# Performance work log

Hardware: AMD Instinct MI355X
Metric: run time of the kernel (lower is better)

Reference implementation:

```python
import jax, jax.numpy as jnp
import numpy as np

NUM_HEADS = 16
HIDDEN = 1024
EPS = 1e-5


def _layer_norm(x, g, b):
    m = jnp.mean(x, axis=-1, keepdims=True)
    v = jnp.mean(jnp.square(x - m), axis=-1, keepdims=True)
    return (x - m) * jax.lax.rsqrt(v + EPS) * g + b


def setup_inputs() -> dict:
    key = jax.random.key(0)
    ks = jax.random.split(key, 6)
    B, S, H = 2, 2048, HIDDEN
    x = jax.random.normal(ks[0], (B, S, H), dtype=jnp.float32)
    # True = masked (original passes ~attn_mask to SDPA); causal mask
    causal = ~jnp.tril(jnp.ones((S, S), dtype=bool))
    attn_mask = causal[None, None, :, :]  # [1,1,S,S]
    sc = 1.0 / np.sqrt(H)
    qkv_w = jax.random.normal(ks[1], (H, 3 * H), dtype=jnp.float32) * sc
    qkv_b = jnp.zeros((3 * H,), dtype=jnp.float32)
    out_w = jax.random.normal(ks[2], (H, H), dtype=jnp.float32) * sc
    out_b = jnp.zeros((H,), dtype=jnp.float32)
    w1 = jax.random.normal(ks[3], (H, 4 * H), dtype=jnp.float32) * sc
    b1 = jnp.zeros((4 * H,), dtype=jnp.float32)
    w2 = jax.random.normal(ks[4], (4 * H, H), dtype=jnp.float32) * (1.0 / np.sqrt(4 * H))
    b2 = jnp.zeros((H,), dtype=jnp.float32)
    return {
        'x': x, 'attn_mask': attn_mask,
        'qkv_w': qkv_w, 'qkv_b': qkv_b, 'out_w': out_w, 'out_b': out_b,
        'w1': w1, 'b1': b1, 'w2': w2, 'b2': b2,
        'ln1_g': jnp.ones((H,), jnp.float32), 'ln1_b': jnp.zeros((H,), jnp.float32),
        'ln2_g': jnp.ones((H,), jnp.float32), 'ln2_b': jnp.zeros((H,), jnp.float32),
    }


def reference(x, attn_mask, qkv_w, qkv_b, out_w, out_b, w1, b1, w2, b2,
              ln1_g, ln1_b, ln2_g, ln2_b):
    B, S, H = x.shape
    nh = NUM_HEADS
    hd = H // nh
    qkv = x @ qkv_w + qkv_b                      # [B,S,3H]
    q, k, v = jnp.split(qkv, 3, axis=-1)
    q = q.reshape(B, S, nh, hd).transpose(0, 2, 1, 3)  # [B,nh,S,hd]
    k = k.reshape(B, S, nh, hd).transpose(0, 2, 1, 3)
    v = v.reshape(B, S, nh, hd).transpose(0, 2, 1, 3)
    scores = jnp.einsum('bhqd,bhkd->bhqk', q, k) / jnp.sqrt(jnp.asarray(hd, x.dtype))
    scores = jnp.where(attn_mask, jnp.finfo(scores.dtype).min, scores)
    p = jax.nn.softmax(scores, axis=-1)
    attn = jnp.einsum('bhqk,bhkd->bhqd', p, v)   # [B,nh,S,hd]
    attn = attn.transpose(0, 2, 1, 3).reshape(B, S, H)
    attn = attn @ out_w + out_b
    x = _layer_norm(x + attn, ln1_g, ln1_b)
    h = jax.nn.relu(x @ w1 + b1) @ w2 + b2
    x = _layer_norm(x + h, ln2_g, ln2_b)
    return x
```

## Files before the change

### kernel.cpp

```cpp
#include <hip/hip_runtime.h>
#include <hip/hip_bf16.h>

typedef __bf16 bf16x8 __attribute__((ext_vector_type(8)));
typedef __bf16 bf16x4 __attribute__((ext_vector_type(4)));
typedef float f32x4 __attribute__((ext_vector_type(4)));

__device__ __forceinline__ void gload16(void* lds, const void* g) {
  __builtin_amdgcn_global_load_lds((const __attribute__((address_space(1))) void*)g,
                                   (__attribute__((address_space(3))) void*)lds, 16, 0, 0);
}

__global__ __launch_bounds__(256)
void transpose_cast(const float* __restrict__ in, __bf16* __restrict__ out, int R, int C)
{
  __shared__ __bf16 tile[32][33];
  const int bc = blockIdx.x * 32, br = blockIdx.y * 32;
  const int lx = threadIdx.x & 31, ly = threadIdx.x >> 5;
#pragma unroll
  for (int p = 0; p < 4; ++p)
    tile[ly + p * 8][lx] = (__bf16)in[(size_t)(br + ly + p * 8) * C + bc + lx];
  __syncthreads();
#pragma unroll
  for (int p = 0; p < 4; ++p)
    out[(size_t)(bc + ly + p * 8) * R + br + lx] = tile[lx][ly + p * 8];
}

__global__ __launch_bounds__(256)
void vtrans(const __bf16* __restrict__ qkv, __bf16* __restrict__ vtg)
{
  __shared__ __bf16 tile[32][33];
  const int sx = blockIdx.x * 32;
  const int dy = blockIdx.y * 32;
  const int z = blockIdx.z;
  const int b = z >> 4, h = z & 15;
  const int lx = threadIdx.x & 31, ly = threadIdx.x >> 5;
  const __bf16* src = qkv + (size_t)b * 2048 * 3072 + 2048 + h * 64;
#pragma unroll
  for (int p = 0; p < 4; ++p)
    tile[ly + p * 8][lx] = src[(size_t)(sx + ly + p * 8) * 3072 + dy + lx];
  __syncthreads();
  __bf16* dst = vtg + (size_t)z * 64 * 2048;
#pragma unroll
  for (int p = 0; p < 4; ++p)
    dst[(size_t)(dy + ly + p * 8) * 2048 + sx + lx] = tile[lx][ly + p * 8];
}

__global__ __launch_bounds__(256)
void cast_bf16(const float* __restrict__ in, __bf16* __restrict__ out)
{
  const int i = (blockIdx.x * 256 + threadIdx.x) * 4;
  float4 v = *(const float4*)(in + i);
  out[i] = (__bf16)v.x; out[i + 1] = (__bf16)v.y;
  out[i + 2] = (__bf16)v.z; out[i + 3] = (__bf16)v.w;
}

template<int BN, bool OUT_BF16, bool RELU, bool RESID>
__global__ __launch_bounds__(256)
void gemm_bt(const __bf16* __restrict__ A, const __bf16* __restrict__ Bt,
             const float* __restrict__ bias, const float* __restrict__ resid,
             void* __restrict__ Cv, int M, int N, int K)
{
  constexpr int NW = BN / 32;
  __shared__ __bf16 As[2][128 * 64];
  __shared__ __bf16 Bs[2][BN * 64];
  const int tid = threadIdx.x;
  const int wave = tid >> 6, lane = tid & 63;
  const int g = lane >> 4, l16 = lane & 15;
  const int row0 = blockIdx.x * 128, col0 = blockIdx.y * BN;
  const int wr = wave >> 1, wc = wave & 1;
  f32x4 acc[4][NW] = {};
  const int nk = K >> 6;

  auto STAGE = [&](int buf, int k0) {
#pragma unroll
    for (int r = 0; r < 4; ++r) {
      const int seg = r * 256 + tid;
      const int arow = seg >> 3;
      const int ko = ((seg & 7) ^ (arow & 7)) * 8;
      gload16(&As[buf][(r * 256 + wave * 64) * 8], &A[(size_t)(row0 + arow) * K + k0 + ko]);
    }
#pragma unroll
    for (int r = 0; r < BN / 32; ++r) {
      const int seg = r * 256 + tid;
      const int brow = seg >> 3;
      const int ko = ((seg & 7) ^ (brow & 7)) * 8;
      gload16(&Bs[buf][(r * 256 + wave * 64) * 8], &Bt[(size_t)(col0 + brow) * K + k0 + ko]);
    }
  };

  STAGE(0, 0);
  __syncthreads();
  int cur = 0;
  for (int t = 0; t < nk; ++t) {
    if (t + 1 < nk) STAGE(cur ^ 1, (t + 1) << 6);
#pragma unroll
    for (int kk = 0; kk < 2; ++kk) {
      bf16x8 af[4], bfr[NW];
#pragma unroll
      for (int m = 0; m < 4; ++m) {
        const int row = wr * 64 + m * 16 + l16;
        af[m] = *(const bf16x8*)&As[cur][row * 64 + ((kk * 32 + g * 8) ^ ((row & 7) << 3))];
      }
#pragma unroll
      for (int n = 0; n < NW; ++n) {
        const int row = wc * (BN / 2) + n * 16 + l16;
        bfr[n] = *(const bf16x8*)&Bs[cur][row * 64 + ((kk * 32 + g * 8) ^ ((row & 7) << 3))];
      }
#pragma unroll
      for (int m = 0; m < 4; ++m)
#pragma unroll
        for (int n = 0; n < NW; ++n)
          acc[m][n] = __builtin_amdgcn_mfma_f32_16x16x32_bf16(af[m], bfr[n], acc[m][n], 0, 0, 0);
    }
    __syncthreads();
    cur ^= 1;
  }
#pragma unroll
  for (int n = 0; n < NW; ++n) {
    const int col = col0 + wc * (BN / 2) + n * 16 + l16;
    const float bv = bias[col];
#pragma unroll
    for (int m = 0; m < 4; ++m) {
      const int rrow = row0 + wr * 64 + m * 16 + g * 4;
#pragma unroll
      for (int r = 0; r < 4; ++r) {
        float v = acc[m][n][r] + bv;
        if (RESID) v += resid[(size_t)(rrow + r) * N + col];
        if (RELU)  v = fmaxf(v, 0.f);
        if (OUT_BF16) ((__bf16*)Cv)[(size_t)(rrow + r) * N + col] = (__bf16)v;
        else          ((float*)Cv)[(size_t)(rrow + r) * N + col] = v;
      }
    }
  }
}

__global__ __launch_bounds__(256)
void attn_fwd(const __bf16* __restrict__ qkv, const __bf16* __restrict__ vtg,
              __bf16* __restrict__ ctx)
{
  constexpr int S = 2048, H = 1024, W3 = 3 * H;
  __shared__ __bf16 Ks[2][64 * 64];
  __shared__ __bf16 Vt[2][64 * 64];
  __shared__ __bf16 Ps[4][16 * 64];
  const int tid = threadIdx.x, wave = tid >> 6, lane = tid & 63;
  const int g = lane >> 4, l16 = lane & 15;
  const int perm = ((l16 & 7) << 1) | (l16 >> 3);
  const int bh = blockIdx.x;
  const int pr = blockIdx.y;
  const int b = bh >> 4, h = bh & 15;
  const size_t base = (size_t)b * S * W3;
  const __bf16* Qg = qkv + base;
  const __bf16* Kg = qkv + base + H;
  const __bf16* Vg = vtg + (size_t)bh * 64 * S;

  auto STAGE_KV = [&](int buf, int kv0) {
#pragma unroll
    for (int r = 0; r < 2; ++r) {
      const int seg = r * 256 + tid;
      const int row = seg >> 3;
      const int ko = ((seg & 7) ^ (row & 7)) * 8;
      gload16(&Ks[buf][(r * 256 + wave * 64) * 8], &Kg[(size_t)(kv0 + row) * W3 + h * 64 + ko]);
      gload16(&Vt[buf][(r * 256 + wave * 64) * 8], &Vg[(size_t)row * S + kv0 + ko]);
    }
  };

#pragma unroll 1
  for (int half = 0; half < 2; ++half) {
    const int qi = half ? (31 - pr) : pr;
    const int q0 = qi * 64;
    const int qrow = q0 + wave * 16 + l16;
    bf16x8 qa[2];
#pragma unroll
    for (int kk = 0; kk < 2; ++kk)
      qa[kk] = *(const bf16x8*)&Qg[(size_t)qrow * W3 + h * 64 + kk * 32 + g * 8];

    f32x4 o[4] = {};
    float lsum = 0.f;
    const int nT = qi + 1;

    STAGE_KV(0, 0);
    __syncthreads();
    int cur = 0;

    for (int t = 0; t < nT; ++t) {
      const int kv0 = t * 64;
      if (t + 1 < nT) STAGE_KV(cur ^ 1, kv0 + 64);

      f32x4 s[4] = {};
      __builtin_amdgcn_s_setprio(1);
#pragma unroll
      for (int kk = 0; kk < 2; ++kk) {
        bf16x8 kb[4];
#pragma unroll
        for (int n = 0; n < 4; ++n) {
          const int row = n * 16 + l16;
          kb[n] = *(const bf16x8*)&Ks[cur][row * 64 + ((kk * 32 + g * 8) ^ ((row & 7) << 3))];
        }
#pragma unroll
        for (int n = 0; n < 4; ++n)
          s[n] = __builtin_amdgcn_mfma_f32_16x16x32_bf16(kb[n], qa[kk], s[n], 0, 0, 0);
      }
      __builtin_amdgcn_s_setprio(0);

      const bool diag = (t == nT - 1);
#pragma unroll
      for (int n = 0; n < 4; ++n) {
        float lp[4];
#pragma unroll
        for (int r = 0; r < 4; ++r) {
          const int ka = kv0 + n * 16 + g * 4 + r;
          float p = exp2f(s[n][r] * 0.18033688f);
          if (diag && ka > qrow) p = 0.f;
          lp[r] = p;
          lsum += p;
        }
        bf16x4 pk;
        pk[0] = (__bf16)lp[0]; pk[1] = (__bf16)lp[1];
        pk[2] = (__bf16)lp[2]; pk[3] = (__bf16)lp[3];
        *(bf16x4*)&Ps[wave][l16 * 64 + (((4 * n + g) ^ perm) << 2)] = pk;
      }

      __builtin_amdgcn_s_setprio(1);
#pragma unroll
      for (int kk = 0; kk < 2; ++kk) {
        const int hb = 8 * kk + 2 * g;
        bf16x4 p0 = *(const bf16x4*)&Ps[wave][l16 * 64 + ((hb ^ perm) << 2)];
        bf16x4 p1 = *(const bf16x4*)&Ps[wave][l16 * 64 + (((hb + 1) ^ perm) << 2)];
        bf16x8 pa = __builtin_shufflevector(p0, p1, 0, 1, 2, 3, 4, 5, 6, 7);
        bf16x8 vb[4];
#pragma unroll
        for (int n2 = 0; n2 < 4; ++n2) {
          const int row = n2 * 16 + l16;
          vb[n2] = *(const bf16x8*)&Vt[cur][row * 64 + ((kk * 32 + g * 8) ^ ((row & 7) << 3))];
        }
#pragma unroll
        for (int n2 = 0; n2 < 4; ++n2)
          o[n2] = __builtin_amdgcn_mfma_f32_16x16x32_bf16(pa, vb[n2], o[n2], 0, 0, 0);
      }
      __builtin_amdgcn_s_setprio(0);
      __syncthreads();
      cur ^= 1;
    }

    lsum += __shfl_xor(lsum, 16);
    lsum += __shfl_xor(lsum, 32);
#pragma unroll
    for (int r = 0; r < 4; ++r) {
      const float den = __shfl(lsum, g * 4 + r);
      const float inv = 1.f / den;
      const int qr = q0 + wave * 16 + g * 4 + r;
#pragma unroll
      for (int n2 = 0; n2 < 4; ++n2) {
        const int d = n2 * 16 + l16;
        ctx[(size_t)(b * S + qr) * H + h * 64 + d] = (__bf16)(o[n2][r] * inv);
      }
    }
  }
}

template<bool WRITE_BF16>
__global__ __launch_bounds__(256)
void ln_kernel(const float* __restrict__ in, const float* __restrict__ gw,
               const float* __restrict__ bw, float* __restrict__ outf,
               __bf16* __restrict__ outb)
{
  const int row = blockIdx.x, tid = threadIdx.x;
  const float4 xv = ((const float4*)(in + (size_t)row * 1024))[tid];
  float s = xv.x + xv.y + xv.z + xv.w;
  float s2 = xv.x * xv.x + xv.y * xv.y + xv.z * xv.z + xv.w * xv.w;
#pragma unroll
  for (int off = 32; off; off >>= 1) { s += __shfl_xor(s, off); s2 += __shfl_xor(s2, off); }
  __shared__ float ps[8];
  if ((tid & 63) == 0) { ps[tid >> 6] = s; ps[4 + (tid >> 6)] = s2; }
  __syncthreads();
  s = ps[0] + ps[1] + ps[2] + ps[3];
  s2 = ps[4] + ps[5] + ps[6] + ps[7];
  const float mean = s * (1.f / 1024.f);
  const float var = s2 * (1.f / 1024.f) - mean * mean;
  const float rs = rsqrtf(var + 1e-5f);
  const float4 gv = ((const float4*)gw)[tid];
  const float4 bv = ((const float4*)bw)[tid];
  float4 y;
  y.x = (xv.x - mean) * rs * gv.x + bv.x;
  y.y = (xv.y - mean) * rs * gv.y + bv.y;
  y.z = (xv.z - mean) * rs * gv.z + bv.z;
  y.w = (xv.w - mean) * rs * gv.w + bv.w;
  ((float4*)(outf + (size_t)row * 1024))[tid] = y;
  if (WRITE_BF16) {
    __bf16* ob = outb + (size_t)row * 1024 + tid * 4;
    ob[0] = (__bf16)y.x; ob[1] = (__bf16)y.y; ob[2] = (__bf16)y.z; ob[3] = (__bf16)y.w;
  }
}

extern "C" void kernel_launch(void* const* d_in, const int* in_sizes, int n_in,
                              void* d_out, int out_size, void* d_ws, size_t ws_size,
                              hipStream_t stream)
{
  (void)in_sizes; (void)n_in; (void)out_size; (void)ws_size;
  const float* x     = (const float*)d_in[0];
  const float* qkv_w = (const float*)d_in[2];
  const float* qkv_b = (const float*)d_in[3];
  const float* out_w = (const float*)d_in[4];
  const float* out_b = (const float*)d_in[5];
  const float* w1    = (const float*)d_in[6];
  const float* b1    = (const float*)d_in[7];
  const float* w2    = (const float*)d_in[8];
  const float* b2    = (const float*)d_in[9];
  const float* ln1g  = (const float*)d_in[10];
  const float* ln1b  = (const float*)d_in[11];
  const float* ln2g  = (const float*)d_in[12];
  const float* ln2b  = (const float*)d_in[13];

  char* ws = (char*)d_ws;
  __bf16* wt_qkv = (__bf16*)(ws + 0);
  __bf16* wt_out = (__bf16*)(ws + 6291456);
  __bf16* wt_w1  = (__bf16*)(ws + 8388608);
  __bf16* wt_w2  = (__bf16*)(ws + 16777216);
  __bf16* xb     = (__bf16*)(ws + 25165824);
  __bf16* big    = (__bf16*)(ws + 33554432);
  float*  res    = (float*)(ws + 67108864);
  float*  x1f    = (float*)(ws + 83886080);
  __bf16* x1b    = (__bf16*)(ws + 100663296);
  __bf16* vtg    = (__bf16*)res;

  transpose_cast<<<dim3(96, 32), 256, 0, stream>>>(qkv_w, wt_qkv, 1024, 3072);
  transpose_cast<<<dim3(32, 32), 256, 0, stream>>>(out_w, wt_out, 1024, 1024);
  transpose_cast<<<dim3(128, 32), 256, 0, stream>>>(w1, wt_w1, 1024, 4096);
  transpose_cast<<<dim3(32, 128), 256, 0, stream>>>(w2, wt_w2, 4096, 1024);
  cast_bf16<<<4096, 256, 0, stream>>>(x, xb);

  gemm_bt<128, true, false, false><<<dim3(32, 24), 256, 0, stream>>>(xb, wt_qkv, qkv_b, nullptr, big, 4096, 3072, 1024);
  vtrans<<<dim3(64, 2, 32), 256, 0, stream>>>(big, vtg);
  attn_fwd<<<dim3(32, 16), 256, 0, stream>>>(big, vtg, xb);
  gemm_bt<64, false, false, true><<<dim3(32, 16), 256, 0, stream>>>(xb, wt_out, out_b, x, res, 4096, 1024, 1024);
  ln_kernel<true><<<4096, 256, 0, stream>>>(res, ln1g, ln1b, x1f, x1b);
  gemm_bt<128, true, true, false><<<dim3(32, 32), 256, 0, stream>>>(x1b, wt_w1, b1, nullptr, big, 4096, 4096, 1024);
  gemm_bt<64, false, false, true><<<dim3(32, 16), 256, 0, stream>>>(big, wt_w2, b2, x1f, res, 4096, 1024, 4096);
  ln_kernel<false><<<4096, 256, 0, stream>>>(res, ln2g, ln2b, (float*)d_out, nullptr);
}
```

Before: 239.9 us.

## Split-K the N=1024 output GEMMs and fold partial sums into layernorm

```diff
diff --git a/kernel.cpp b/kernel.cpp
--- a/kernel.cpp
+++ b/kernel.cpp
@@ -129,6 +129,82 @@
         if (RELU)  v = fmaxf(v, 0.f);
         if (OUT_BF16) ((__bf16*)Cv)[(size_t)(rrow + r) * N + col] = (__bf16)v;
         else          ((float*)Cv)[(size_t)(rrow + r) * N + col] = v;
+      }
+    }
+  }
+}
+
+template<bool RESID>
+__global__ __launch_bounds__(256)
+void gemm_splitk(const __bf16* __restrict__ A, const __bf16* __restrict__ Bt,
+                 const float* __restrict__ bias, const float* __restrict__ resid,
+                 float* __restrict__ C0, float* __restrict__ C1,
+                 int M, int N, int Kfull, int Ksub)
+{
+  __shared__ __bf16 As[2][128 * 64];
+  __shared__ __bf16 Bs[2][128 * 64];
+  const int tid = threadIdx.x;
+  const int wave = tid >> 6, lane = tid & 63;
+  const int g = lane >> 4, l16 = lane & 15;
+  const int row0 = blockIdx.x * 128, col0 = blockIdx.y * 128;
+  const int z = blockIdx.z;
+  const __bf16* Az = A + (size_t)z * Ksub;
+  const __bf16* Bz = Bt + (size_t)z * Ksub;
+  float* C = z ? C1 : C0;
+  const int wr = wave >> 1, wc = wave & 1;
+  f32x4 acc[4][4] = {};
+  const int nk = Ksub >> 6;
+
+  auto STAGE = [&](int buf, int k0) {
+#pragma unroll
+    for (int r = 0; r < 4; ++r) {
+      const int seg = r * 256 + tid;
+      const int arow = seg >> 3;
+      const int ko = ((seg & 7) ^ (arow & 7)) * 8;
+      gload16(&As[buf][(r * 256 + wave * 64) * 8], &Az[(size_t)(row0 + arow) * Kfull + k0 + ko]);
+      gload16(&Bs[buf][(r * 256 + wave * 64) * 8], &Bz[(size_t)(col0 + arow) * Kfull + k0 + ko]);
+    }
+  };
+
+  STAGE(0, 0);
+  __syncthreads();
+  int cur = 0;
+  for (int t = 0; t < nk; ++t) {
+    if (t + 1 < nk) STAGE(cur ^ 1, (t + 1) << 6);
+#pragma unroll
+    for (int kk = 0; kk < 2; ++kk) {
+      bf16x8 af[4], bfr[4];
+#pragma unroll
+      for (int m = 0; m < 4; ++m) {
+        const int row = wr * 64 + m * 16 + l16;
+        af[m] = *(const bf16x8*)&As[cur][row * 64 + ((kk * 32 + g * 8) ^ ((row & 7) << 3))];
+      }
+#pragma unroll
+      for (int n = 0; n < 4; ++n) {
+        const int row = wc * 64 + n * 16 + l16;
+        bfr[n] = *(const bf16x8*)&Bs[cur][row * 64 + ((kk * 32 + g * 8) ^ ((row & 7) << 3))];
+      }
+#pragma unroll
+      for (int m = 0; m < 4; ++m)
+#pragma unroll
+        for (int n = 0; n < 4; ++n)
+          acc[m][n] = __builtin_amdgcn_mfma_f32_16x16x32_bf16(af[m], bfr[n], acc[m][n], 0, 0, 0);
+    }
+    __syncthreads();
+    cur ^= 1;
+  }
+#pragma unroll
+  for (int n = 0; n < 4; ++n) {
+    const int col = col0 + wc * 64 + n * 16 + l16;
+    const float bv = (z == 0) ? bias[col] : 0.f;
+#pragma unroll
+    for (int m = 0; m < 4; ++m) {
+      const int rrow = row0 + wr * 64 + m * 16 + g * 4;
+#pragma unroll
+      for (int r = 0; r < 4; ++r) {
+        float v = acc[m][n][r] + bv;
+        if (RESID) { if (z == 0) v += resid[(size_t)(rrow + r) * N + col]; }
+        C[(size_t)(rrow + r) * N + col] = v;
       }
     }
   }
@@ -166,7 +242,7 @@
 
 #pragma unroll 1
   for (int half = 0; half < 2; ++half) {
-    const int qi = half ? (31 - pr) : pr;
+    const int qi = half ? (31 - blockIdx.y) : blockIdx.y;
     const int q0 = qi * 64;
     const int qrow = q0 + wave * 16 + l16;
     bf16x8 qa[2];
@@ -258,14 +334,18 @@
   }
 }
 
-template<bool WRITE_BF16>
-__global__ __launch_bounds__(256)
-void ln_kernel(const float* __restrict__ in, const float* __restrict__ gw,
-               const float* __restrict__ bw, float* __restrict__ outf,
-               __bf16* __restrict__ outb)
+template<bool WRITE_BF16, bool TWO_IN>
+__global__ __launch_bounds__(256)
+void ln_kernel(const float* __restrict__ in, const float* __restrict__ in2,
+               const float* __restrict__ gw, const float* __restrict__ bw,
+               float* __restrict__ outf, __bf16* __restrict__ outb)
 {
   const int row = blockIdx.x, tid = threadIdx.x;
-  const float4 xv = ((const float4*)(in + (size_t)row * 1024))[tid];
+  float4 xv = ((const float4*)(in + (size_t)row * 1024))[tid];
+  if (TWO_IN) {
+    const float4 yv = ((const float4*)(in2 + (size_t)row * 1024))[tid];
+    xv.x += yv.x; xv.y += yv.y; xv.z += yv.z; xv.w += yv.w;
+  }
   float s = xv.x + xv.y + xv.z + xv.w;
   float s2 = xv.x * xv.x + xv.y * xv.y + xv.z * xv.z + xv.w * xv.w;
 #pragma unroll
@@ -322,6 +402,8 @@
   float*  x1f    = (float*)(ws + 83886080);
   __bf16* x1b    = (__bf16*)(ws + 100663296);
   __bf16* vtg    = (__bf16*)res;
+  float*  pB     = (float*)big;
+  float*  qB     = (float*)ws;
 
   transpose_cast<<<dim3(96, 32), 256, 0, stream>>>(qkv_w, wt_qkv, 1024, 3072);
   transpose_cast<<<dim3(32, 32), 256, 0, stream>>>(out_w, wt_out, 1024, 1024);
@@ -332,9 +414,9 @@
   gemm_bt<128, true, false, false><<<dim3(32, 24), 256, 0, stream>>>(xb, wt_qkv, qkv_b, nullptr, big, 4096, 3072, 1024);
   vtrans<<<dim3(64, 2, 32), 256, 0, stream>>>(big, vtg);
   attn_fwd<<<dim3(32, 16), 256, 0, stream>>>(big, vtg, xb);
-  gemm_bt<64, false, false, true><<<dim3(32, 16), 256, 0, stream>>>(xb, wt_out, out_b, x, res, 4096, 1024, 1024);
-  ln_kernel<true><<<4096, 256, 0, stream>>>(res, ln1g, ln1b, x1f, x1b);
+  gemm_splitk<true><<<dim3(32, 8, 2), 256, 0, stream>>>(xb, wt_out, out_b, x, res, pB, 4096, 1024, 1024, 512);
+  ln_kernel<true, true><<<4096, 256, 0, stream>>>(res, pB, ln1g, ln1b, x1f, x1b);
   gemm_bt<128, true, true, false><<<dim3(32, 32), 256, 0, stream>>>(x1b, wt_w1, b1, nullptr, big, 4096, 4096, 1024);
-  gemm_bt<64, false, false, true><<<dim3(32, 16), 256, 0, stream>>>(big, wt_w2, b2, x1f, res, 4096, 1024, 4096);
-  ln_kernel<false><<<4096, 256, 0, stream>>>(res, ln2g, ln2b, (float*)d_out, nullptr);
-}
+  gemm_splitk<true><<<dim3(32, 8, 2), 256, 0, stream>>>(big, wt_w2, b2, x1f, res, qB, 4096, 1024, 4096, 2048);
+  ln_kernel<false, true><<<4096, 256, 0, stream>>>(res, qB, ln2g, ln2b, (float*)d_out, nullptr);
+}
```

Result: slower. 246.7 us (+2.8%).

## Replace GEMM with 512-thread 4-stage pipelined kernel and split-K for narrow GEMMs

Applied to the files above, without the earlier changes.

```diff
diff --git a/kernel.cpp b/kernel.cpp
--- a/kernel.cpp
+++ b/kernel.cpp
@@ -54,81 +54,120 @@
   out[i + 2] = (__bf16)v.z; out[i + 3] = (__bf16)v.w;
 }
 
-template<int BN, bool OUT_BF16, bool RELU, bool RESID>
-__global__ __launch_bounds__(256)
-void gemm_bt(const __bf16* __restrict__ A, const __bf16* __restrict__ Bt,
-             const float* __restrict__ bias, const float* __restrict__ resid,
-             void* __restrict__ Cv, int M, int N, int K)
-{
-  constexpr int NW = BN / 32;
-  __shared__ __bf16 As[2][128 * 64];
-  __shared__ __bf16 Bs[2][BN * 64];
-  const int tid = threadIdx.x;
-  const int wave = tid >> 6, lane = tid & 63;
+template<int BM, bool OUTBF16, bool RELU, bool RESID, bool SPLIT>
+__global__ __launch_bounds__(512, 2)
+void gemm8(const __bf16* __restrict__ A, const __bf16* __restrict__ Bt,
+           const float* __restrict__ bias, const float* __restrict__ resid,
+           void* __restrict__ C0v, void* __restrict__ C1v,
+           int M, int N, int Kfull, int Ksub)
+{
+  constexpr int FM = BM / 32;
+  constexpr int RA = BM / 128;
+  __shared__ __align__(16) __bf16 As[4][BM * 32];
+  __shared__ __align__(16) __bf16 Bs[4][256 * 32];
+  const int tid = threadIdx.x, wave = tid >> 6, lane = tid & 63;
   const int g = lane >> 4, l16 = lane & 15;
-  const int row0 = blockIdx.x * 128, col0 = blockIdx.y * BN;
-  const int wr = wave >> 1, wc = wave & 1;
-  f32x4 acc[4][NW] = {};
-  const int nk = K >> 6;
-
-  auto STAGE = [&](int buf, int k0) {
-#pragma unroll
-    for (int r = 0; r < 4; ++r) {
-      const int seg = r * 256 + tid;
-      const int arow = seg >> 3;
-      const int ko = ((seg & 7) ^ (arow & 7)) * 8;
-      gload16(&As[buf][(r * 256 + wave * 64) * 8], &A[(size_t)(row0 + arow) * K + k0 + ko]);
-    }
-#pragma unroll
-    for (int r = 0; r < BN / 32; ++r) {
-      const int seg = r * 256 + tid;
-      const int brow = seg >> 3;
-      const int ko = ((seg & 7) ^ (brow & 7)) * 8;
-      gload16(&Bs[buf][(r * 256 + wave * 64) * 8], &Bt[(size_t)(col0 + brow) * K + k0 + ko]);
+  const int wr = wave >> 2, wc = wave & 3;
+  const int row0 = blockIdx.x * BM, col0 = blockIdx.y * 256;
+  const int z = SPLIT ? blockIdx.z : 0;
+  const __bf16* Az = A + (size_t)z * Ksub;
+  const __bf16* Bz = Bt + (size_t)z * Ksub;
+  const int nk = Ksub >> 5;
+  const int wbase = wave * 64;
+  f32x4 acc[FM][4] = {};
+
+  auto STAGE = [&](int buf, int ks) {
+    const int k0 = ks << 5;
+#pragma unroll
+    for (int r = 0; r < RA; ++r) {
+      const int seg = r * 512 + tid;
+      const int row = seg >> 2;
+      const int src = ((seg & 3) ^ ((row >> 1) & 3)) << 3;
+      gload16(&As[buf][(size_t)(r * 512 + wbase) * 8],
+              &Az[(size_t)(row0 + row) * Kfull + k0 + src]);
+    }
+#pragma unroll
+    for (int r = 0; r < 2; ++r) {
+      const int seg = r * 512 + tid;
+      const int row = seg >> 2;
+      const int src = ((seg & 3) ^ ((row >> 1) & 3)) << 3;
+      gload16(&Bs[buf][(size_t)(r * 512 + wbase) * 8],
+              &Bz[(size_t)(col0 + row) * Kfull + k0 + src]);
     }
   };
 
-  STAGE(0, 0);
-  __syncthreads();
-  int cur = 0;
+  STAGE(0, 0); STAGE(1, 1); STAGE(2, 2);
+
+#pragma unroll 1
   for (int t = 0; t < nk; ++t) {
-    if (t + 1 < nk) STAGE(cur ^ 1, (t + 1) << 6);
-#pragma unroll
-    for (int kk = 0; kk < 2; ++kk) {
-      bf16x8 af[4], bfr[NW];
-#pragma unroll
-      for (int m = 0; m < 4; ++m) {
-        const int row = wr * 64 + m * 16 + l16;
-        af[m] = *(const bf16x8*)&As[cur][row * 64 + ((kk * 32 + g * 8) ^ ((row & 7) << 3))];
-      }
-#pragma unroll
-      for (int n = 0; n < NW; ++n) {
-        const int row = wc * (BN / 2) + n * 16 + l16;
-        bfr[n] = *(const bf16x8*)&Bs[cur][row * 64 + ((kk * 32 + g * 8) ^ ((row & 7) << 3))];
-      }
-#pragma unroll
-      for (int m = 0; m < 4; ++m)
-#pragma unroll
-        for (int n = 0; n < NW; ++n)
-          acc[m][n] = __builtin_amdgcn_mfma_f32_16x16x32_bf16(af[m], bfr[n], acc[m][n], 0, 0, 0);
-    }
-    __syncthreads();
-    cur ^= 1;
-  }
-#pragma unroll
-  for (int n = 0; n < NW; ++n) {
-    const int col = col0 + wc * (BN / 2) + n * 16 + l16;
-    const float bv = bias[col];
-#pragma unroll
-    for (int m = 0; m < 4; ++m) {
-      const int rrow = row0 + wr * 64 + m * 16 + g * 4;
-#pragma unroll
-      for (int r = 0; r < 4; ++r) {
-        float v = acc[m][n][r] + bv;
-        if (RESID) v += resid[(size_t)(rrow + r) * N + col];
-        if (RELU)  v = fmaxf(v, 0.f);
-        if (OUT_BF16) ((__bf16*)Cv)[(size_t)(rrow + r) * N + col] = (__bf16)v;
-        else          ((float*)Cv)[(size_t)(rrow + r) * N + col] = v;
+    const int cur = t & 3;
+    const int nxt = (t + 3 < nk) ? (t + 3) : (nk - 1);
+    STAGE((t + 3) & 3, nxt);
+    if constexpr (BM == 256) asm volatile("s_waitcnt vmcnt(12)" ::: "memory");
+    else                     asm volatile("s_waitcnt vmcnt(9)" ::: "memory");
+    __builtin_amdgcn_s_barrier();
+    asm volatile("" ::: "memory");
+
+    bf16x8 bfr[4];
+#pragma unroll
+    for (int fn = 0; fn < 4; ++fn) {
+      const int row = wc * 64 + fn * 16 + l16;
+      bfr[fn] = *(const bf16x8*)&Bs[cur][row * 32 + ((g ^ ((row >> 1) & 3)) << 3)];
+    }
+    bf16x8 af[FM / 2];
+#pragma unroll
+    for (int fm = 0; fm < FM / 2; ++fm) {
+      const int row = wr * (BM / 2) + fm * 16 + l16;
+      af[fm] = *(const bf16x8*)&As[cur][row * 32 + ((g ^ ((row >> 1) & 3)) << 3)];
+    }
+    __builtin_amdgcn_s_setprio(1);
+#pragma unroll
+    for (int fm = 0; fm < FM / 2; ++fm)
+#pragma unroll
+      for (int fn = 0; fn < 4; ++fn)
+        acc[fm][fn] = __builtin_amdgcn_mfma_f32_16x16x32_bf16(af[fm], bfr[fn], acc[fm][fn], 0, 0, 0);
+    __builtin_amdgcn_s_setprio(0);
+
+    bf16x8 af2[FM / 2];
+#pragma unroll
+    for (int fm = 0; fm < FM / 2; ++fm) {
+      const int row = wr * (BM / 2) + (FM / 2 + fm) * 16 + l16;
+      af2[fm] = *(const bf16x8*)&As[cur][row * 32 + ((g ^ ((row >> 1) & 3)) << 3)];
+    }
+    __builtin_amdgcn_s_setprio(1);
+#pragma unroll
+    for (int fm = 0; fm < FM / 2; ++fm)
+#pragma unroll
+      for (int fn = 0; fn < 4; ++fn)
+        acc[FM / 2 + fm][fn] = __builtin_amdgcn_mfma_f32_16x16x32_bf16(af2[fm], bfr[fn], acc[FM / 2 + fm][fn], 0, 0, 0);
+    __builtin_amdgcn_s_setprio(0);
+
+    asm volatile("s_waitcnt lgkmcnt(0)" ::: "memory");
+    __builtin_amdgcn_s_barrier();
+    asm volatile("" ::: "memory");
+  }
+
+#pragma unroll
+  for (int fn = 0; fn < 4; ++fn) {
+    const int col = col0 + wc * 64 + fn * 16 + l16;
+    float bv = 0.f;
+    if (!SPLIT || z == 0) bv = bias[col];
+#pragma unroll
+    for (int fm = 0; fm < FM; ++fm) {
+      const int rbase = row0 + wr * (BM / 2) + fm * 16 + g * 4;
+#pragma unroll
+      for (int j = 0; j < 4; ++j) {
+        float v = acc[fm][fn][j] + bv;
+        if (RESID) { if (!SPLIT || z == 0) v += resid[(size_t)(rbase + j) * N + col]; }
+        if (RELU) v = fmaxf(v, 0.f);
+        if (SPLIT) {
+          float* C = z ? (float*)C1v : (float*)C0v;
+          C[(size_t)(rbase + j) * N + col] = v;
+        } else if (OUTBF16) {
+          ((__bf16*)C0v)[(size_t)(rbase + j) * N + col] = (__bf16)v;
+        } else {
+          ((float*)C0v)[(size_t)(rbase + j) * N + col] = v;
+        }
       }
     }
   }
@@ -146,7 +185,6 @@
   const int g = lane >> 4, l16 = lane & 15;
   const int perm = ((l16 & 7) << 1) | (l16 >> 3);
   const int bh = blockIdx.x;
-  const int pr = blockIdx.y;
   const int b = bh >> 4, h = bh & 15;
   const size_t base = (size_t)b * S * W3;
   const __bf16* Qg = qkv + base;
@@ -166,7 +204,7 @@
 
 #pragma unroll 1
   for (int half = 0; half < 2; ++half) {
-    const int qi = half ? (31 - pr) : pr;
+    const int qi = half ? (31 - blockIdx.y) : blockIdx.y;
     const int q0 = qi * 64;
     const int qrow = q0 + wave * 16 + l16;
     bf16x8 qa[2];
@@ -258,14 +296,18 @@
   }
 }
 
-template<bool WRITE_BF16>
-__global__ __launch_bounds__(256)
-void ln_kernel(const float* __restrict__ in, const float* __restrict__ gw,
-               const float* __restrict__ bw, float* __restrict__ outf,
-               __bf16* __restrict__ outb)
+template<bool WRITE_BF16, bool TWO_IN>
+__global__ __launch_bounds__(256)
+void ln_kernel(const float* __restrict__ in, const float* __restrict__ in2,
+               const float* __restrict__ gw, const float* __restrict__ bw,
+               float* __restrict__ outf, __bf16* __restrict__ outb)
 {
   const int row = blockIdx.x, tid = threadIdx.x;
-  const float4 xv = ((const float4*)(in + (size_t)row * 1024))[tid];
+  float4 xv = ((const float4*)(in + (size_t)row * 1024))[tid];
+  if (TWO_IN) {
+    const float4 yv = ((const float4*)(in2 + (size_t)row * 1024))[tid];
+    xv.x += yv.x; xv.y += yv.y; xv.z += yv.z; xv.w += yv.w;
+  }
   float s = xv.x + xv.y + xv.z + xv.w;
   float s2 = xv.x * xv.x + xv.y * xv.y + xv.z * xv.z + xv.w * xv.w;
 #pragma unroll
@@ -322,6 +364,8 @@
   float*  x1f    = (float*)(ws + 83886080);
   __bf16* x1b    = (__bf16*)(ws + 100663296);
   __bf16* vtg    = (__bf16*)res;
+  float*  pB     = (float*)big;
+  float*  qB     = (float*)ws;
 
   transpose_cast<<<dim3(96, 32), 256, 0, stream>>>(qkv_w, wt_qkv, 1024, 3072);
   transpose_cast<<<dim3(32, 32), 256, 0, stream>>>(out_w, wt_out, 1024, 1024);
@@ -329,12 +373,16 @@
   transpose_cast<<<dim3(32, 128), 256, 0, stream>>>(w2, wt_w2, 4096, 1024);
   cast_bf16<<<4096, 256, 0, stream>>>(x, xb);
 
-  gemm_bt<128, true, false, false><<<dim3(32, 24), 256, 0, stream>>>(xb, wt_qkv, qkv_b, nullptr, big, 4096, 3072, 1024);
+  gemm8<256, true, false, false, false><<<dim3(16, 12, 1), 512, 0, stream>>>(
+      xb, wt_qkv, qkv_b, nullptr, big, nullptr, 4096, 3072, 1024, 1024);
   vtrans<<<dim3(64, 2, 32), 256, 0, stream>>>(big, vtg);
   attn_fwd<<<dim3(32, 16), 256, 0, stream>>>(big, vtg, xb);
-  gemm_bt<64, false, false, true><<<dim3(32, 16), 256, 0, stream>>>(xb, wt_out, out_b, x, res, 4096, 1024, 1024);
-  ln_kernel<true><<<4096, 256, 0, stream>>>(res, ln1g, ln1b, x1f, x1b);
-  gemm_bt<128, true, true, false><<<dim3(32, 32), 256, 0, stream>>>(x1b, wt_w1, b1, nullptr, big, 4096, 4096, 1024);
-  gemm_bt<64, false, false, true><<<dim3(32, 16), 256, 0, stream>>>(big, wt_w2, b2, x1f, res, 4096, 1024, 4096);
-  ln_kernel<false><<<4096, 256, 0, stream>>>(res, ln2g, ln2b, (float*)d_out, nullptr);
-}
+  gemm8<128, false, false, true, true><<<dim3(32, 4, 2), 512, 0, stream>>>(
+      xb, wt_out, out_b, x, res, pB, 4096, 1024, 1024, 512);
+  ln_kernel<true, true><<<4096, 256, 0, stream>>>(res, pB, ln1g, ln1b, x1f, x1b);
+  gemm8<256, true, true, false, false><<<dim3(16, 16, 1), 512, 0, stream>>>(
+      x1b, wt_w1, b1, nullptr, big, nullptr, 4096, 4096, 1024, 1024);
+  gemm8<128, false, false, true, true><<<dim3(32, 4, 2), 512, 0, stream>>>(
+      big, wt_w2, b2, x1f, res, qB, 4096, 1024, 4096, 2048);
+  ln_kernel<false, true><<<4096, 256, 0, stream>>>(res, qB, ln2g, ln2b, (float*)d_out, nullptr);
+}
```

Measured after the change: 286.0 us. 1.19x slower.

## Use BK=32 GEMM tiles and split-K the FFN down-projection into two partials

Applied to the files above, without the earlier changes.

```diff
diff --git a/kernel.cpp b/kernel.cpp
--- a/kernel.cpp
+++ b/kernel.cpp
@@ -54,37 +54,44 @@
   out[i + 2] = (__bf16)v.z; out[i + 3] = (__bf16)v.w;
 }
 
-template<int BN, bool OUT_BF16, bool RELU, bool RESID>
+template<int BN, int BK, bool OUT_BF16, bool RELU, bool RESID, bool SPLIT>
 __global__ __launch_bounds__(256)
 void gemm_bt(const __bf16* __restrict__ A, const __bf16* __restrict__ Bt,
              const float* __restrict__ bias, const float* __restrict__ resid,
-             void* __restrict__ Cv, int M, int N, int K)
+             void* __restrict__ C0v, float* __restrict__ C1,
+             int M, int N, int Kfull, int Ksub)
 {
   constexpr int NW = BN / 32;
-  __shared__ __bf16 As[2][128 * 64];
-  __shared__ __bf16 Bs[2][BN * 64];
+  constexpr int CH = BK / 8;
+  __shared__ __bf16 As[2][128 * BK];
+  __shared__ __bf16 Bs[2][BN * BK];
   const int tid = threadIdx.x;
   const int wave = tid >> 6, lane = tid & 63;
   const int g = lane >> 4, l16 = lane & 15;
   const int row0 = blockIdx.x * 128, col0 = blockIdx.y * BN;
+  const int z = SPLIT ? blockIdx.z : 0;
+  const __bf16* Az = A + (size_t)z * Ksub;
+  const __bf16* Bz = Bt + (size_t)z * Ksub;
   const int wr = wave >> 1, wc = wave & 1;
   f32x4 acc[4][NW] = {};
-  const int nk = K >> 6;
+  const int nk = Ksub / BK;
+
+  auto KEY = [](int row) -> int { return (BK == 64) ? (row & 7) : ((row >> 1) & 3); };
 
   auto STAGE = [&](int buf, int k0) {
 #pragma unroll
-    for (int r = 0; r < 4; ++r) {
+    for (int r = 0; r < 128 * CH / 256; ++r) {
       const int seg = r * 256 + tid;
-      const int arow = seg >> 3;
-      const int ko = ((seg & 7) ^ (arow & 7)) * 8;
-      gload16(&As[buf][(r * 256 + wave * 64) * 8], &A[(size_t)(row0 + arow) * K + k0 + ko]);
-    }
-#pragma unroll
-    for (int r = 0; r < BN / 32; ++r) {
+      const int row = seg / CH, cp = seg % CH;
+      const int src = (cp ^ KEY(row)) * 8;
+      gload16(&As[buf][(r * 256 + wave * 64) * 8], &Az[(size_t)(row0 + row) * Kfull + k0 + src]);
+    }
+#pragma unroll
+    for (int r = 0; r < BN * CH / 256; ++r) {
       const int seg = r * 256 + tid;
-      const int brow = seg >> 3;
-      const int ko = ((seg & 7) ^ (brow & 7)) * 8;
-      gload16(&Bs[buf][(r * 256 + wave * 64) * 8], &Bt[(size_t)(col0 + brow) * K + k0 + ko]);
+      const int row = seg / CH, cp = seg % CH;
+      const int src = (cp ^ KEY(row)) * 8;
+      gload16(&Bs[buf][(r * 256 + wave * 64) * 8], &Bz[(size_t)(col0 + row) * Kfull + k0 + src]);
     }
   };
 
@@ -92,19 +99,19 @@
   __syncthreads();
   int cur = 0;
   for (int t = 0; t < nk; ++t) {
-    if (t + 1 < nk) STAGE(cur ^ 1, (t + 1) << 6);
-#pragma unroll
-    for (int kk = 0; kk < 2; ++kk) {
+    if (t + 1 < nk) STAGE(cur ^ 1, (t + 1) * BK);
+#pragma unroll
+    for (int kk = 0; kk < BK / 32; ++kk) {
       bf16x8 af[4], bfr[NW];
 #pragma unroll
       for (int m = 0; m < 4; ++m) {
         const int row = wr * 64 + m * 16 + l16;
-        af[m] = *(const bf16x8*)&As[cur][row * 64 + ((kk * 32 + g * 8) ^ ((row & 7) << 3))];
+        af[m] = *(const bf16x8*)&As[cur][row * BK + (((kk * 4 + g) ^ KEY(row)) << 3)];
       }
 #pragma unroll
       for (int n = 0; n < NW; ++n) {
         const int row = wc * (BN / 2) + n * 16 + l16;
-        bfr[n] = *(const bf16x8*)&Bs[cur][row * 64 + ((kk * 32 + g * 8) ^ ((row & 7) << 3))];
+        bfr[n] = *(const bf16x8*)&Bs[cur][row * BK + (((kk * 4 + g) ^ KEY(row)) << 3)];
       }
 #pragma unroll
       for (int m = 0; m < 4; ++m)
@@ -118,17 +125,25 @@
 #pragma unroll
   for (int n = 0; n < NW; ++n) {
     const int col = col0 + wc * (BN / 2) + n * 16 + l16;
-    const float bv = bias[col];
+    float bv = 0.f;
+    if (!SPLIT || z == 0) bv = bias[col];
 #pragma unroll
     for (int m = 0; m < 4; ++m) {
       const int rrow = row0 + wr * 64 + m * 16 + g * 4;
 #pragma unroll
       for (int r = 0; r < 4; ++r) {
         float v = acc[m][n][r] + bv;
-        if (RESID) v += resid[(size_t)(rrow + r) * N + col];
-        if (RELU)  v = fmaxf(v, 0.f);
-        if (OUT_BF16) ((__bf16*)Cv)[(size_t)(rrow + r) * N + col] = (__bf16)v;
-        else          ((float*)Cv)[(size_t)(rrow + r) * N + col] = v;
+        const size_t idx = (size_t)(rrow + r) * N + col;
+        if (SPLIT) {
+          if (RESID) { if (z == 0) v += resid[idx]; }
+          float* C = z ? C1 : (float*)C0v;
+          C[idx] = v;
+        } else {
+          if (RESID) v += resid[idx];
+          if (RELU)  v = fmaxf(v, 0.f);
+          if (OUT_BF16) ((__bf16*)C0v)[idx] = (__bf16)v;
+          else          ((float*)C0v)[idx] = v;
+        }
       }
     }
   }
@@ -146,7 +161,6 @@
   const int g = lane >> 4, l16 = lane & 15;
   const int perm = ((l16 & 7) << 1) | (l16 >> 3);
   const int bh = blockIdx.x;
-  const int pr = blockIdx.y;
   const int b = bh >> 4, h = bh & 15;
   const size_t base = (size_t)b * S * W3;
   const __bf16* Qg = qkv + base;
@@ -166,7 +180,7 @@
 
 #pragma unroll 1
   for (int half = 0; half < 2; ++half) {
-    const int qi = half ? (31 - pr) : pr;
+    const int qi = half ? (31 - blockIdx.y) : blockIdx.y;
     const int q0 = qi * 64;
     const int qrow = q0 + wave * 16 + l16;
     bf16x8 qa[2];
@@ -258,14 +272,18 @@
   }
 }
 
-template<bool WRITE_BF16>
-__global__ __launch_bounds__(256)
-void ln_kernel(const float* __restrict__ in, const float* __restrict__ gw,
-               const float* __restrict__ bw, float* __restrict__ outf,
-               __bf16* __restrict__ outb)
+template<bool WRITE_BF16, bool TWO_IN>
+__global__ __launch_bounds__(256)
+void ln_kernel(const float* __restrict__ in, const float* __restrict__ in2,
+               const float* __restrict__ gw, const float* __restrict__ bw,
+               float* __restrict__ outf, __bf16* __restrict__ outb)
 {
   const int row = blockIdx.x, tid = threadIdx.x;
-  const float4 xv = ((const float4*)(in + (size_t)row * 1024))[tid];
+  float4 xv = ((const float4*)(in + (size_t)row * 1024))[tid];
+  if (TWO_IN) {
+    const float4 yv = ((const float4*)(in2 + (size_t)row * 1024))[tid];
+    xv.x += yv.x; xv.y += yv.y; xv.z += yv.z; xv.w += yv.w;
+  }
   float s = xv.x + xv.y + xv.z + xv.w;
   float s2 = xv.x * xv.x + xv.y * xv.y + xv.z * xv.z + xv.w * xv.w;
 #pragma unroll
@@ -322,6 +340,7 @@
   float*  x1f    = (float*)(ws + 83886080);
   __bf16* x1b    = (__bf16*)(ws + 100663296);
   __bf16* vtg    = (__bf16*)res;
+  float*  qB     = (float*)ws;
 
   transpose_cast<<<dim3(96, 32), 256, 0, stream>>>(qkv_w, wt_qkv, 1024, 3072);
   transpose_cast<<<dim3(32, 32), 256, 0, stream>>>(out_w, wt_out, 1024, 1024);
@@ -329,12 +348,16 @@
   transpose_cast<<<dim3(32, 128), 256, 0, stream>>>(w2, wt_w2, 4096, 1024);
   cast_bf16<<<4096, 256, 0, stream>>>(x, xb);
 
-  gemm_bt<128, true, false, false><<<dim3(32, 24), 256, 0, stream>>>(xb, wt_qkv, qkv_b, nullptr, big, 4096, 3072, 1024);
+  gemm_bt<128, 32, true, false, false, false><<<dim3(32, 24), 256, 0, stream>>>(
+      xb, wt_qkv, qkv_b, nullptr, big, nullptr, 4096, 3072, 1024, 1024);
   vtrans<<<dim3(64, 2, 32), 256, 0, stream>>>(big, vtg);
   attn_fwd<<<dim3(32, 16), 256, 0, stream>>>(big, vtg, xb);
-  gemm_bt<64, false, false, true><<<dim3(32, 16), 256, 0, stream>>>(xb, wt_out, out_b, x, res, 4096, 1024, 1024);
-  ln_kernel<true><<<4096, 256, 0, stream>>>(res, ln1g, ln1b, x1f, x1b);
-  gemm_bt<128, true, true, false><<<dim3(32, 32), 256, 0, stream>>>(x1b, wt_w1, b1, nullptr, big, 4096, 4096, 1024);
-  gemm_bt<64, false, false, true><<<dim3(32, 16), 256, 0, stream>>>(big, wt_w2, b2, x1f, res, 4096, 1024, 4096);
-  ln_kernel<false><<<4096, 256, 0, stream>>>(res, ln2g, ln2b, (float*)d_out, nullptr);
-}
+  gemm_bt<64, 32, false, false, true, false><<<dim3(32, 16), 256, 0, stream>>>(
+      xb, wt_out, out_b, x, res, nullptr, 4096, 1024, 1024, 1024);
+  ln_kernel<true, false><<<4096, 256, 0, stream>>>(res, nullptr, ln1g, ln1b, x1f, x1b);
+  gemm_bt<128, 32, true, true, false, false><<<dim3(32, 32), 256, 0, stream>>>(
+      x1b, wt_w1, b1, nullptr, big, nullptr, 4096, 4096, 1024, 1024);
+  gemm_bt<128, 32, false, false, true, true><<<dim3(32, 8, 2), 256, 0, stream>>>(
+      big, wt_w2, b2, x1f, res, qB, 4096, 1024, 4096, 2048);
+  ln_kernel<false, true><<<4096, 256, 0, stream>>>(res, qB, ln2g, ln2b, (float*)d_out, nullptr);
+}
```

After: 250.4 us. +4.4%, slower.
